# Kernel optimization log

Measured on AMD Instinct MI355X. Metric: run time of the kernel, lower is better.

Reference implementation:

```python
import jax, jax.numpy as jnp
import numpy as np


def _conv3x3(x, w):
    # NCHW input, OIHW weight, stride 1, padding 1 (SAME for 3x3)
    return jax.lax.conv_general_dilated(
        x, w, window_strides=(1, 1), padding=((1, 1), (1, 1)),
        dimension_numbers=('NCHW', 'OIHW', 'NCHW'))


def _conv1x1(x, w):
    return jax.lax.conv_general_dilated(
        x, w, window_strides=(1, 1), padding=((0, 0), (0, 0)),
        dimension_numbers=('NCHW', 'OIHW', 'NCHW'))


def setup_inputs() -> dict:
    key = jax.random.key(0)
    k_x, k_w1, k_w2, k_wm = jax.random.split(key, 4)
    N, C, H, W = 16, 256, 64, 64
    fan = C * 9
    x = jax.random.normal(k_x, (N, C, H, W), dtype=jnp.float32)
    w1 = jax.random.normal(k_w1, (C, C, 3, 3), dtype=jnp.float32) * (2.0 / fan) ** 0.5
    w2 = jax.random.normal(k_w2, (C, C, 3, 3), dtype=jnp.float32) * (2.0 / fan) ** 0.5
    w_mask = jax.random.normal(k_wm, (1, C, 1, 1), dtype=jnp.float32) * (1.0 / C) ** 0.5
    b_mask = jnp.zeros((1,), dtype=jnp.float32)
    return {'x': x, 'w1': w1, 'w2': w2, 'w_mask': w_mask, 'b_mask': b_mask}


def reference(x, w1, w2, w_mask, b_mask):
    # MaskUnit: 1x1 conv -> logits -> hard binary mask (straight-through estimator)
    logits = _conv1x1(x, w_mask) + b_mask[None, :, None, None]  # [N,1,H,W]
    hard = (logits > 0).astype(x.dtype)
    mask = logits + jax.lax.stop_gradient(hard - logits)        # std mask, binary in fwd
    # dilated mask: 3x3 max-pool (covers 3x3 receptive field of active outputs)
    mask_dilate = jax.lax.reduce_window(
        mask, -jnp.inf, jax.lax.max, (1, 1, 3, 3), (1, 1, 1, 1), 'SAME')
    # sparse branch: conv1 gated by dilated mask, conv2 gated by std mask
    h = jax.nn.relu(_conv3x3(x, w1) * mask_dilate)
    h = jax.nn.relu(_conv3x3(h, w2) * mask)
    # apply_mask + residual (mask binary -> h*mask == h already, kept for fidelity)
    out = x + h * mask
    return out
```

## Files before the change

kernel.cpp:

```cpp
#include <hip/hip_runtime.h>
#include <hip/hip_bf16.h>

#define C_ 256
#define H_ 64
#define W_ 64
#define N_ 16
#define HW_ 4096
#define IMG_ (C_ * HW_)
#define PADIMG_ (66 * 66 * 256)
#define WT_ELEMS_ (9 * 256 * 256)

typedef short bf16x8 __attribute__((ext_vector_type(8)));
typedef float f32x16 __attribute__((ext_vector_type(16)));

__device__ __forceinline__ unsigned short f2bf(float f) {
  __hip_bfloat16 h = __float2bfloat16(f);
  return *reinterpret_cast<unsigned short*>(&h);
}

__device__ __forceinline__ void gld_lds16(const void* g, void* l) {
  __builtin_amdgcn_global_load_lds(
      (const __attribute__((address_space(1))) void*)g,
      (__attribute__((address_space(3))) void*)l, 16, 0, 0);
}

__global__ __launch_bounds__(256) void xpadmask_kernel(
    const float* __restrict__ x, const float* __restrict__ wm,
    const float* __restrict__ bm, short* __restrict__ Xp,
    unsigned char* __restrict__ mask) {
  __shared__ unsigned short lds[64 * 260];
  __shared__ float wms[256];
  __shared__ double sums[4][64];
  const int h = blockIdx.x, img = blockIdx.y;
  const int tid = threadIdx.x;
  const int wv = tid >> 6, wl = tid & 63;
  wms[tid] = wm[tid];
  __syncthreads();
  const float* xi = x + (size_t)img * IMG_ + h * 64;
  double a0 = 0.0, a1 = 0.0, a2 = 0.0, a3 = 0.0;
#pragma unroll 4
  for (int i = 0; i < 16; ++i) {
#pragma unroll
    for (int u = 0; u < 4; ++u) {
      int c = (i * 4 + u) * 4 + wv;
      float v = xi[(size_t)c * HW_ + wl];
      lds[wl * 260 + c] = f2bf(v);
      double p = (double)v * (double)wms[c];
      if (u == 0) a0 += p;
      else if (u == 1) a1 += p;
      else if (u == 2) a2 += p;
      else a3 += p;
    }
  }
  sums[wv][wl] = (a0 + a1) + (a2 + a3);
  __syncthreads();
  short* Xpi = Xp + (size_t)img * PADIMG_ + ((h + 1) * 66 + 1) * 256;
#pragma unroll
  for (int j = 0; j < 16; ++j) {
    int w = j * 4 + wv;
    int c4 = wl * 4;
    uint2 d = *(const uint2*)&lds[w * 260 + c4];
    *(uint2*)&Xpi[(size_t)w * 256 + c4] = d;
  }
  if (wv == 0) {
    double t = sums[0][wl] + sums[1][wl] + sums[2][wl] + sums[3][wl] +
               (double)bm[0];
    mask[img * HW_ + h * 64 + wl] = (t > 0.0) ? 1 : 0;
  }
}

__global__ __launch_bounds__(256) void dilate_kernel(
    const unsigned char* __restrict__ mask, unsigned char* __restrict__ md) {
  int pix = blockIdx.x * 256 + threadIdx.x;
  int n = pix >> 12;
  int hw = pix & (HW_ - 1);
  int h = hw >> 6, w = hw & 63;
  int m = 0;
  for (int dy = -1; dy <= 1; dy++) {
    int hh = h + dy;
    if (hh < 0 || hh >= H_) continue;
    for (int dx = -1; dx <= 1; dx++) {
      int ww = w + dx;
      if (ww < 0 || ww >= W_) continue;
      m |= mask[n * HW_ + hh * W_ + ww];
    }
  }
  md[pix] = (unsigned char)m;
}

__global__ __launch_bounds__(256) void wt_kernel(
    const float* __restrict__ w1, const float* __restrict__ w2,
    short* __restrict__ Wt1, short* __restrict__ Wt2) {
  const int k = blockIdx.x, c = threadIdx.x;
  const float* src = blockIdx.y ? w2 : w1;
  short* dst = blockIdx.y ? Wt2 : Wt1;
  const float* s = src + ((size_t)k * 256 + c) * 9;
#pragma unroll
  for (int t = 0; t < 9; ++t)
    dst[t * 65536 + k * 256 + c] = (short)f2bf(s[t]);
}

__global__ __launch_bounds__(128) void halo_zero(short* __restrict__ Xp,
                                                 short* __restrict__ Hp) {
  int p = blockIdx.x;
  int r, c;
  if (p < 66) { r = 0; c = p; }
  else if (p < 132) { r = 65; c = p - 66; }
  else if (p < 196) { r = p - 131; c = 0; }
  else { r = p - 195; c = 65; }
  short* buf = blockIdx.z ? Hp : Xp;
  unsigned int* d = (unsigned int*)(buf + (size_t)blockIdx.y * PADIMG_ +
                                    (size_t)(r * 66 + c) * 256);
  d[threadIdx.x] = 0u;
}

#define BREG 5280
#define WBASE 21120
#define WREG 4608

__device__ __forceinline__ void stage_tile(short* sm, const short* Xb,
                                           const short* Wt, int ch0, int buf,
                                           int ko, int wave, int lane) {
  short* Bd = sm + buf * 2 * BREG;
  short* Wd = sm + WBASE + buf * 2 * WREG;
#pragma unroll
  for (int q = 0; q < 6; ++q) {
    int n = wave + 4 * q;
    if (n > 21) n = 21;
    const int h = (n >= 11) ? 1 : 0;
    const int i = n - h * 11;
    const int row0 = (i < 10) ? i * 64 : 596;
    gld_lds16(Xb + (size_t)(row0 + lane) * 256 + ko + h * 8,
              Bd + h * BREG + row0 * 8);
  }
#pragma unroll
  for (int q = 0; q < 5; ++q) {
    int n = wave + 4 * q;
    if (n > 17) n = 17;
    const int h = (n >= 9) ? 1 : 0;
    const int t = n - h * 9;
    gld_lds16(Wt + (size_t)t * 65536 + (size_t)(ch0 + lane) * 256 + ko + h * 8,
              Wd + h * WREG + t * 512);
  }
}

template <int EPI>
__global__ __launch_bounds__(256, 2) void conv_mfma(
    const short* __restrict__ src, const short* __restrict__ Wt,
    const unsigned char* __restrict__ gate, const float* __restrict__ xres,
    short* __restrict__ dstH, float* __restrict__ dstF, int swz) {
  __shared__ __align__(16) short sm[39552];

  const int tid = threadIdx.x;
  const int lane = tid & 63, wave = tid >> 6;
  const int ln31 = lane & 31, kh = lane >> 5;

  int bx, by, bz;
  {
    int d = blockIdx.x + 4 * (blockIdx.y + 8 * blockIdx.z);
    if (swz) {
      int k = d & 7, j = d >> 3;
      bx = j & 3;
      by = (j >> 2) & 7;
      bz = ((j >> 5) << 3) + k;
    } else {
      bx = blockIdx.x;
      by = blockIdx.y;
      bz = blockIdx.z;
    }
  }
  const int ch0 = bx * 64;
  const int h0 = by * 8;
  const int img = bz;

  const short* Xb = src + (size_t)img * PADIMG_ + (size_t)(h0 * 66) * 256;

  f32x16 acc[2][4];
#pragma unroll
  for (int i = 0; i < 2; ++i)
#pragma unroll
    for (int j = 0; j < 4; ++j)
#pragma unroll
      for (int e = 0; e < 16; ++e) acc[i][j][e] = 0.f;

  stage_tile(sm, Xb, Wt, ch0, 0, 0, wave, lane);
  asm volatile("s_waitcnt vmcnt(0)\n\ts_barrier" ::: "memory");

#pragma unroll 2
  for (int kk = 0; kk < 16; ++kk) {
    const int cur = kk & 1;
    if (kk < 15) stage_tile(sm, Xb, Wt, ch0, cur ^ 1, (kk + 1) * 16, wave, lane);

    const short* Bth = sm + (cur * 2 + kh) * BREG + (wave * 132 + ln31) * 8;
    const short* Wth = sm + WBASE + (cur * 2 + kh) * WREG + ln31 * 8;
#pragma unroll
    for (int t = 0; t < 9; ++t) {
      const int dy = t / 3, dx = t % 3;
      bf16x8 a0 = *(const bf16x8*)(Wth + t * 512);
      bf16x8 a1 = *(const bf16x8*)(Wth + t * 512 + 256);
      bf16x8 b[4];
#pragma unroll
      for (int j = 0; j < 4; ++j) {
        const int off = (((j >> 1) + dy) * 66 + (j & 1) * 32 + dx) * 8;
        b[j] = *(const bf16x8*)(Bth + off);
      }
#pragma unroll
      for (int j = 0; j < 4; ++j) {
        acc[0][j] = __builtin_amdgcn_mfma_f32_32x32x16_bf16(a0, b[j],
                                                            acc[0][j], 0, 0, 0);
        acc[1][j] = __builtin_amdgcn_mfma_f32_32x32x16_bf16(a1, b[j],
                                                            acc[1][j], 0, 0, 0);
      }
    }
    if (kk < 15)
      asm volatile("s_waitcnt vmcnt(0)\n\ts_barrier" ::: "memory");
  }

  const int rb = h0 + wave * 2;
#pragma unroll
  for (int j = 0; j < 4; ++j) {
    const int r = rb + (j >> 1);
    const int col = (j & 1) * 32 + ln31;
    const int pidx = r * 64 + col;
    const unsigned char g = gate[img * HW_ + pidx];
#pragma unroll
    for (int i = 0; i < 2; ++i) {
      const f32x16 v = acc[i][j];
#pragma unroll
      for (int rg = 0; rg < 4; ++rg) {
        const int ch = ch0 + i * 32 + rg * 8 + kh * 4;
        float e0 = g ? fmaxf(v[rg * 4 + 0], 0.f) : 0.f;
        float e1 = g ? fmaxf(v[rg * 4 + 1], 0.f) : 0.f;
        float e2 = g ? fmaxf(v[rg * 4 + 2], 0.f) : 0.f;
        float e3 = g ? fmaxf(v[rg * 4 + 3], 0.f) : 0.f;
        if (EPI == 0) {
          uint2 u;
          u.x = (unsigned int)f2bf(e0) | ((unsigned int)f2bf(e1) << 16);
          u.y = (unsigned int)f2bf(e2) | ((unsigned int)f2bf(e3) << 16);
          short* dp = dstH + (size_t)img * PADIMG_ +
                      ((size_t)((r + 1) * 66 + (col + 1))) * 256 + ch;
          *(uint2*)dp = u;
        } else {
          size_t o = (size_t)img * IMG_ + (size_t)ch * HW_ + pidx;
          dstF[o] = xres[o] + e0;
          dstF[o + HW_] = xres[o + HW_] + e1;
          dstF[o + 2 * HW_] = xres[o + 2 * HW_] + e2;
          dstF[o + 3 * HW_] = xres[o + 3 * HW_] + e3;
        }
      }
    }
  }
}

extern "C" void kernel_launch(void* const* d_in, const int* in_sizes, int n_in,
                              void* d_out, int out_size, void* d_ws,
                              size_t ws_size, hipStream_t stream) {
  const float* x = (const float*)d_in[0];
  const float* w1 = (const float*)d_in[1];
  const float* w2 = (const float*)d_in[2];
  const float* wmask = (const float*)d_in[3];
  const float* bmask = (const float*)d_in[4];
  float* out = (float*)d_out;

  char* ws = (char*)d_ws;
  unsigned char* mask = (unsigned char*)ws;
  unsigned char* md = (unsigned char*)(ws + 65536);
  short* Wt1 = (short*)(ws + 131072);
  short* Wt2 = Wt1 + WT_ELEMS_;
  short* Xp = (short*)(ws + 2490368);

  const size_t fixed = 2490368;
  const size_t tailpad = 32768;
  const size_t per_img = 2 * (size_t)PADIMG_ * 2;
  int B = (ws_size > fixed + tailpad)
              ? (int)((ws_size - fixed - tailpad) / per_img) : 0;
  if (B > N_) B = N_;
  if (B < 1) B = 1;
  short* Hp = Xp + (size_t)B * PADIMG_;

  wt_kernel<<<dim3(256, 2), 256, 0, stream>>>(w1, w2, Wt1, Wt2);
  halo_zero<<<dim3(260, B, 2), 128, 0, stream>>>(Xp, Hp);

  for (int n0 = 0; n0 < N_; n0 += B) {
    const int nb = (N_ - n0 < B) ? (N_ - n0) : B;
    const int swz = (nb % 8 == 0) ? 1 : 0;
    xpadmask_kernel<<<dim3(64, nb), 256, 0, stream>>>(
        x + (size_t)n0 * IMG_, wmask, bmask, Xp, mask + n0 * HW_);
    dilate_kernel<<<nb * HW_ / 256, 256, 0, stream>>>(mask + n0 * HW_,
                                                      md + n0 * HW_);
    conv_mfma<0><<<dim3(4, 8, nb), 256, 0, stream>>>(
        Xp, Wt1, md + n0 * HW_, nullptr, Hp, nullptr, swz);
    conv_mfma<1><<<dim3(4, 8, nb), 256, 0, stream>>>(
        Hp, Wt2, mask + n0 * HW_, x + (size_t)n0 * IMG_, nullptr,
        out + (size_t)n0 * IMG_, swz);
  }
}
```

Measured before the change: 330.3 us.

## Stream conv weights from global into registers and triple-buffer input tiles in LDS

Result: faster. 299.7 us (-9.3%).

```diff
diff --git a/kernel.cpp b/kernel.cpp
--- a/kernel.cpp
+++ b/kernel.cpp
@@ -95,9 +95,10 @@
   const float* src = blockIdx.y ? w2 : w1;
   short* dst = blockIdx.y ? Wt2 : Wt1;
   const float* s = src + ((size_t)k * 256 + c) * 9;
+  const int kc = c >> 4, ce = c & 15;
 #pragma unroll
   for (int t = 0; t < 9; ++t)
-    dst[t * 65536 + k * 256 + c] = (short)f2bf(s[t]);
+    dst[(((size_t)t * 16 + kc) * 256 + k) * 16 + ce] = (short)f2bf(s[t]);
 }
 
 __global__ __launch_bounds__(128) void halo_zero(short* __restrict__ Xp,
@@ -114,15 +115,11 @@
   d[threadIdx.x] = 0u;
 }
 
-#define BREG 5280
-#define WBASE 21120
-#define WREG 4608
-
-__device__ __forceinline__ void stage_tile(short* sm, const short* Xb,
-                                           const short* Wt, int ch0, int buf,
-                                           int ko, int wave, int lane) {
-  short* Bd = sm + buf * 2 * BREG;
-  short* Wd = sm + WBASE + buf * 2 * WREG;
+#define BBUF 10560
+
+__device__ __forceinline__ void stage_B(short* sm, int buf, const short* Xb,
+                                        int ko, int wave, int lane) {
+  short* Bd = sm + buf * BBUF;
 #pragma unroll
   for (int q = 0; q < 6; ++q) {
     int n = wave + 4 * q;
@@ -131,16 +128,7 @@
     const int i = n - h * 11;
     const int row0 = (i < 10) ? i * 64 : 596;
     gld_lds16(Xb + (size_t)(row0 + lane) * 256 + ko + h * 8,
-              Bd + h * BREG + row0 * 8);
-  }
-#pragma unroll
-  for (int q = 0; q < 5; ++q) {
-    int n = wave + 4 * q;
-    if (n > 17) n = 17;
-    const int h = (n >= 9) ? 1 : 0;
-    const int t = n - h * 9;
-    gld_lds16(Wt + (size_t)t * 65536 + (size_t)(ch0 + lane) * 256 + ko + h * 8,
-              Wd + h * WREG + t * 512);
+              Bd + h * 5280 + row0 * 8);
   }
 }
 
@@ -149,7 +137,7 @@
     const short* __restrict__ src, const short* __restrict__ Wt,
     const unsigned char* __restrict__ gate, const float* __restrict__ xres,
     short* __restrict__ dstH, float* __restrict__ dstF, int swz) {
-  __shared__ __align__(16) short sm[39552];
+  __shared__ __align__(16) short sm[3 * BBUF];
 
   const int tid = threadIdx.x;
   const int lane = tid & 63, wave = tid >> 6;
@@ -174,6 +162,7 @@
   const int img = bz;
 
   const short* Xb = src + (size_t)img * PADIMG_ + (size_t)(h0 * 66) * 256;
+  const short* WL = Wt + ((size_t)(ch0 + ln31)) * 16 + kh * 8;
 
   f32x16 acc[2][4];
 #pragma unroll
@@ -183,37 +172,45 @@
 #pragma unroll
       for (int e = 0; e < 16; ++e) acc[i][j][e] = 0.f;
 
-  stage_tile(sm, Xb, Wt, ch0, 0, 0, wave, lane);
-  asm volatile("s_waitcnt vmcnt(0)\n\ts_barrier" ::: "memory");
-
-#pragma unroll 2
+  stage_B(sm, 0, Xb, 0, wave, lane);
+  bf16x8 wa0 = *(const bf16x8*)(WL);
+  bf16x8 wa1 = *(const bf16x8*)(WL + 512);
+  stage_B(sm, 1, Xb, 16, wave, lane);
+  asm volatile("s_waitcnt vmcnt(6)\n\ts_barrier" ::: "memory");
+
+  int c0 = 0, c1 = 1, c2 = 2;
   for (int kk = 0; kk < 16; ++kk) {
-    const int cur = kk & 1;
-    if (kk < 15) stage_tile(sm, Xb, Wt, ch0, cur ^ 1, (kk + 1) * 16, wave, lane);
-
-    const short* Bth = sm + (cur * 2 + kh) * BREG + (wave * 132 + ln31) * 8;
-    const short* Wth = sm + WBASE + (cur * 2 + kh) * WREG + ln31 * 8;
+    const short* Bth = sm + c0 * BBUF + kh * 5280 + (wave * 132 + ln31) * 8;
 #pragma unroll
     for (int t = 0; t < 9; ++t) {
+      const int ntkc = (t < 8) ? ((t + 1) * 16 + kk) : (kk + 1);
+      bf16x8 na0 = *(const bf16x8*)(WL + (size_t)ntkc * 4096);
+      bf16x8 na1 = *(const bf16x8*)(WL + (size_t)ntkc * 4096 + 512);
       const int dy = t / 3, dx = t % 3;
-      bf16x8 a0 = *(const bf16x8*)(Wth + t * 512);
-      bf16x8 a1 = *(const bf16x8*)(Wth + t * 512 + 256);
       bf16x8 b[4];
 #pragma unroll
       for (int j = 0; j < 4; ++j) {
         const int off = (((j >> 1) + dy) * 66 + (j & 1) * 32 + dx) * 8;
         b[j] = *(const bf16x8*)(Bth + off);
       }
+      __builtin_amdgcn_s_setprio(1);
 #pragma unroll
       for (int j = 0; j < 4; ++j) {
-        acc[0][j] = __builtin_amdgcn_mfma_f32_32x32x16_bf16(a0, b[j],
+        acc[0][j] = __builtin_amdgcn_mfma_f32_32x32x16_bf16(wa0, b[j],
                                                             acc[0][j], 0, 0, 0);
-        acc[1][j] = __builtin_amdgcn_mfma_f32_32x32x16_bf16(a1, b[j],
+        acc[1][j] = __builtin_amdgcn_mfma_f32_32x32x16_bf16(wa1, b[j],
                                                             acc[1][j], 0, 0, 0);
       }
-    }
-    if (kk < 15)
-      asm volatile("s_waitcnt vmcnt(0)\n\ts_barrier" ::: "memory");
+      __builtin_amdgcn_s_setprio(0);
+      wa0 = na0;
+      wa1 = na1;
+    }
+    if (kk < 14) stage_B(sm, c2, Xb, (kk + 2) * 16, wave, lane);
+    if (kk < 15) asm volatile("s_barrier" ::: "memory");
+    const int tmp = c0;
+    c0 = c1;
+    c1 = c2;
+    c2 = tmp;
   }
 
   const int rb = h0 + wave * 2;
```
